# Optimization experiments

Hardware: AMD Instinct MI355X
Metric: run time of the kernel (lower is better)

Reference implementation:

```python
import jax, jax.numpy as jnp
import numpy as np


def setup_inputs() -> dict:
    key = jax.random.key(0)
    k1, k2, k3 = jax.random.split(key, 3)
    N, D, H, E = 8192, 1024, 1024, 16
    scale = 1.0 / np.sqrt(D)
    return {
        "x": jax.random.normal(k1, (N, D), dtype=jnp.float32),
        "router_w": jax.random.normal(k2, (D, E), dtype=jnp.float32) * scale,
        "router_b": jnp.zeros((E,), dtype=jnp.float32),
        "expert_w": jax.random.normal(k3, (E, D, H), dtype=jnp.float32) * scale,
        "expert_b": jnp.zeros((E, H), dtype=jnp.float32),
        "k": 2,
    }


def reference(x, router_w, router_b, expert_w, expert_b, k):
    # Router: softmax over experts, then top-k.
    logits = x @ router_w + router_b                      # [N, E]
    routing_weights = jax.nn.softmax(logits, axis=-1)     # [N, E]
    top_k_weights, top_k_indices = jax.lax.top_k(routing_weights, k)  # [N, k]

    # Dense all-expert compute (faithful to original): [N, E, H]
    expert_outputs = jnp.einsum('nd,edh->neh', x, expert_w) + expert_b[None, :, :]

    # Gather top-k expert outputs: [N, k, H]
    gathered = jnp.take_along_axis(expert_outputs, top_k_indices[:, :, None], axis=1)

    # Weighted sum over k (weights NOT renormalized, as in the original).
    out = jnp.sum(top_k_weights[:, :, None] * gathered, axis=1)  # [N, H]
    return out
```

## Files before the change

kernel.cpp:

```cpp
#include <hip/hip_runtime.h>
#include <hip/hip_bf16.h>


#define N_TOK 8192
#define D_DIM 1024
#define H_DIM 1024
#define E_NUM 16
#define CAP   1024
#define KPAD  40

typedef __attribute__((ext_vector_type(4))) float f32x4;
typedef __attribute__((ext_vector_type(8))) short bf16x8;

__device__ __forceinline__ unsigned short f2bf(float f) {
    unsigned int u = __float_as_uint(f);
    unsigned int r = u + 0x7fffu + ((u >> 16) & 1u);
    return (unsigned short)(r >> 16);
}
__device__ __forceinline__ unsigned int pk2bf(float lo, float hi) {
    return (unsigned int)f2bf(lo) | ((unsigned int)f2bf(hi) << 16);
}

__global__ __launch_bounds__(256, 4) void router_kernel(
    const float* __restrict__ x,
    const float* __restrict__ rw,
    const float* __restrict__ rb,
    int4* __restrict__ res)
{
    const int wave = threadIdx.x >> 6;
    const int lane = threadIdx.x & 63;
    const int ds   = lane >> 4;
    const int e    = lane & 15;
    const int t0   = blockIdx.x * 8 + wave * 2;

    const float* x0  = x + (size_t)t0 * D_DIM + ds * 256;
    const float* x1  = x0 + D_DIM;
    const float* rwp = rw + ds * 4096 + e;

    double acc0 = 0.0, acc1 = 0.0;
#pragma unroll 2
    for (int g = 0; g < 8; ++g) {
        float s0 = 0.0f, s1 = 0.0f;
#pragma unroll
        for (int u = 0; u < 8; ++u) {
            const int jb = g * 8 + u;
            const float4 a = *(const float4*)(x0 + jb * 4);
            const float4 b = *(const float4*)(x1 + jb * 4);
            const float w0 = rwp[jb * 64];
            const float w1 = rwp[jb * 64 + 16];
            const float w2 = rwp[jb * 64 + 32];
            const float w3 = rwp[jb * 64 + 48];
            s0 = fmaf(a.w, w3, fmaf(a.z, w2, fmaf(a.y, w1, fmaf(a.x, w0, s0))));
            s1 = fmaf(b.w, w3, fmaf(b.z, w2, fmaf(b.y, w1, fmaf(b.x, w0, s1))));
        }
        acc0 += (double)s0;
        acc1 += (double)s1;
    }

    double v0 = acc0, v1 = acc1;
    v0 += __shfl_xor(v0, 16); v0 += __shfl_xor(v0, 32);
    v1 += __shfl_xor(v1, 16); v1 += __shfl_xor(v1, 32);

    __shared__ double lg[4][2][E_NUM];
    if (ds == 0) {
        const double bias = (double)rb[e];
        lg[wave][0][e] = v0 + bias;
        lg[wave][1][e] = v1 + bias;
    }
    __syncthreads();

    if (lane < 2) {
        const double* L = lg[wave][lane];
        double m = L[0];
#pragma unroll
        for (int k = 1; k < E_NUM; ++k) m = fmax(m, L[k]);

        int e1 = 0;
#pragma unroll
        for (int k = 1; k < E_NUM; ++k) if (L[k] > L[e1]) e1 = k;
        int e2 = (e1 == 0) ? 1 : 0;
        for (int k = 0; k < E_NUM; ++k)
            if (k != e1 && L[k] > L[e2]) e2 = k;

        float s = 0.0f;
#pragma unroll
        for (int k = 0; k < E_NUM; ++k) s = fmaf(expf((float)(L[k] - m)), 1.0f, s);
        const float w1 = expf((float)(L[e1] - m)) / s;
        const float w2 = expf((float)(L[e2] - m)) / s;

        const int n = t0 + lane;
        res[n] = make_int4(e1, e2, __float_as_int(w1), __float_as_int(w2));
    }
}

__global__ __launch_bounds__(256) void build_lists(
    const int4* __restrict__ res,
    int* __restrict__ counts0, int* __restrict__ counts1,
    int2* __restrict__ entries0, int2* __restrict__ entries1)
{
    const int e = blockIdx.x;
    __shared__ int c0, c1;
    if (threadIdx.x == 0) { c0 = 0; c1 = 0; }
    __syncthreads();

    for (int i = threadIdx.x; i < N_TOK; i += 256) {
        const int4 r = res[i];
        if (r.x == e) {
            int p = atomicAdd(&c0, 1);
            if (p < CAP) entries0[e * CAP + p] = make_int2(i, r.z);
        }
        if (r.y == e) {
            int p = atomicAdd(&c1, 1);
            if (p < CAP) entries1[e * CAP + p] = make_int2(i, r.w);
        }
    }
    __syncthreads();
    if (threadIdx.x == 0) { counts0[e] = c0; counts1[e] = c1; }
}

__global__ __launch_bounds__(256) void cvt_kernel(
    const float* __restrict__ x,
    const float* __restrict__ ew,
    unsigned short* __restrict__ xb,
    unsigned short* __restrict__ wt)
{
    const int tid = threadIdx.x;
    if (blockIdx.x < 4096) {
        const size_t base = ((size_t)blockIdx.x * 256 + tid) * 8;
        const float4 a = *(const float4*)(x + base);
        const float4 b = *(const float4*)(x + base + 4);
        uint4 p;
        p.x = pk2bf(a.x, a.y); p.y = pk2bf(a.z, a.w);
        p.z = pk2bf(b.x, b.y); p.w = pk2bf(b.z, b.w);
        *(uint4*)(xb + base) = p;
        return;
    }
    __shared__ unsigned short Ts[64][68];
    const int wi = blockIdx.x - 4096;
    const int e  = wi >> 8;
    const int kt = (wi >> 4) & 15;
    const int ht = wi & 15;

    {
        const int kl0 = tid >> 4;
        const int hl  = (tid & 15) * 4;
        const float* src = ew + (size_t)e * (D_DIM * H_DIM)
                         + (size_t)(kt * 64 + kl0) * H_DIM + ht * 64 + hl;
#pragma unroll
        for (int i = 0; i < 4; ++i) {
            const float4 v = *(const float4*)(src + (size_t)i * 16 * H_DIM);
            ushort4 p;
            p.x = f2bf(v.x); p.y = f2bf(v.y); p.z = f2bf(v.z); p.w = f2bf(v.w);
            *(ushort4*)&Ts[kl0 + i * 16][hl] = p;
        }
    }
    __syncthreads();
    {
        const int h2 = tid >> 2;
        const int kc = (tid & 3) * 16;
        unsigned int r[8];
#pragma unroll
        for (int i = 0; i < 8; ++i)
            r[i] = (unsigned int)Ts[kc + 2 * i][h2]
                 | ((unsigned int)Ts[kc + 2 * i + 1][h2] << 16);
        unsigned short* dst = wt + (size_t)e * (D_DIM * H_DIM)
                            + (size_t)(ht * 64 + h2) * D_DIM + kt * 64 + kc;
        *(uint4*)dst       = *(uint4*)&r[0];
        *(uint4*)(dst + 8) = *(uint4*)&r[4];
    }
}

template <bool ADD>
__global__ __launch_bounds__(256) void moe_gemm_bf16(
    const unsigned short* __restrict__ xb,
    const unsigned short* __restrict__ wt,
    const float* __restrict__ eb,
    const int* __restrict__ counts,
    const int2* __restrict__ entries,
    float* __restrict__ out)
{
    int e = 0, loc = blockIdx.x, count = 0;
    for (; e < E_NUM; ++e) {
        int c = counts[e]; if (c > CAP) c = CAP;
        const int nb = ((c + 127) >> 7) << 3;
        if (loc < nb) { count = c; break; }
        loc -= nb;
    }
    if (e == E_NUM) return;
    const int i0 = (loc >> 3) * 128;
    const int h0 = (loc & 7) * 128;

    __shared__ unsigned short Xs[2][128][KPAD];
    __shared__ unsigned short Ws[2][128][KPAD];
    __shared__ int   s_tok[128];
    __shared__ float s_w[128];

    const int tid = threadIdx.x;
    if (tid < 128) {
        const int i = i0 + tid;
        if (i < count) {
            int2 en = entries[e * CAP + i];
            s_tok[tid] = en.x;
            s_w[tid] = __int_as_float(en.y);
        } else {
            s_tok[tid] = 0;
            s_w[tid] = 0.0f;
        }
    }
    __syncthreads();

    const int wave = tid >> 6;
    const int lane = tid & 63;
    const int wr = (wave >> 1) * 64;
    const int wc = (wave & 1) * 64;
    const int l15 = lane & 15;
    const int quad = lane >> 4;

    f32x4 acc[4][4] = {};

    const int row  = tid >> 1;
    const int half = (tid & 1) * 16;
    const unsigned short* xp = xb + (size_t)s_tok[row] * D_DIM + half;
    const unsigned short* wp = wt + (size_t)(e * H_DIM + h0 + row) * D_DIM + half;

    uint4 pa0 = *(const uint4*)(xp);
    uint4 pa1 = *(const uint4*)(xp + 8);
    uint4 pw0 = *(const uint4*)(wp);
    uint4 pw1 = *(const uint4*)(wp + 8);
    *(uint4*)&Xs[0][row][half]     = pa0;
    *(uint4*)&Xs[0][row][half + 8] = pa1;
    *(uint4*)&Ws[0][row][half]     = pw0;
    *(uint4*)&Ws[0][row][half + 8] = pw1;

    int cur = 0;
    for (int d0 = 0; d0 < D_DIM; d0 += 32) {
        __syncthreads();
        const bool more = (d0 + 32 < D_DIM);

        if (more) {
            pa0 = *(const uint4*)(xp + d0 + 32);
            pa1 = *(const uint4*)(xp + d0 + 40);
            pw0 = *(const uint4*)(wp + d0 + 32);
            pw1 = *(const uint4*)(wp + d0 + 40);
        }

        bf16x8 af[4], bq[4];
#pragma unroll
        for (int i = 0; i < 4; ++i)
            af[i] = *(const bf16x8*)&Xs[cur][wr + i * 16 + l15][quad * 8];
#pragma unroll
        for (int j = 0; j < 4; ++j)
            bq[j] = *(const bf16x8*)&Ws[cur][wc + j * 16 + l15][quad * 8];
#pragma unroll
        for (int i = 0; i < 4; ++i)
#pragma unroll
            for (int j = 0; j < 4; ++j)
                acc[i][j] = __builtin_amdgcn_mfma_f32_16x16x32_bf16(
                    af[i], bq[j], acc[i][j], 0, 0, 0);

        if (more) {
            const int nxt = cur ^ 1;
            *(uint4*)&Xs[nxt][row][half]     = pa0;
            *(uint4*)&Xs[nxt][row][half + 8] = pa1;
            *(uint4*)&Ws[nxt][row][half]     = pw0;
            *(uint4*)&Ws[nxt][row][half + 8] = pw1;
        }
        cur ^= 1;
    }

    float bias_j[4];
    const float* ebp = eb + e * H_DIM + h0 + wc;
#pragma unroll
    for (int j = 0; j < 4; ++j) bias_j[j] = ebp[j * 16 + l15];

#pragma unroll
    for (int i = 0; i < 4; ++i) {
#pragma unroll
        for (int r = 0; r < 4; ++r) {
            const int orow = wr + i * 16 + quad * 4 + r;
            if (i0 + orow < count) {
                const int tok = s_tok[orow];
                const float w = s_w[orow];
                float* op = out + (size_t)tok * H_DIM + h0 + wc + l15;
#pragma unroll
                for (int j = 0; j < 4; ++j) {
                    float v = w * (acc[i][j][r] + bias_j[j]);
                    if (ADD) v += op[j * 16];
                    op[j * 16] = v;
                }
            }
        }
    }
}

template <bool ADD>
__global__ __launch_bounds__(256) void moe_mfma_kernel(
    const float* __restrict__ x,
    const float* __restrict__ ew,
    const float* __restrict__ eb,
    const int* __restrict__ counts,
    const int2* __restrict__ entries,
    float* __restrict__ out)
{
    const int flat = blockIdx.x;
    const int lid  = (flat & 7) * 128 + (flat >> 3);
    const int h0 = (lid & 7) * 128;
    const int i0 = ((lid >> 3) & 7) * 128;
    const int e  = lid >> 6;

    int count = counts[e];
    if (count > CAP) count = CAP;
    if (i0 >= count) return;

    __shared__ unsigned short Xs[2][128][KPAD];
    __shared__ unsigned short Ws[2][128][KPAD];
    __shared__ int   s_tok[128];
    __shared__ float s_w[128];

    const int tid = threadIdx.x;
    if (tid < 128) {
        const int i = i0 + tid;
        if (i < count) {
            int2 en = entries[e * CAP + i];
            s_tok[tid] = en.x;
            s_w[tid] = __int_as_float(en.y);
        } else {
            s_tok[tid] = 0;
            s_w[tid] = 0.0f;
        }
    }
    __syncthreads();

    const int wave = tid >> 6;
    const int lane = tid & 63;
    const int wr = (wave >> 1) * 64;
    const int wc = (wave & 1) * 64;
    const int l15 = lane & 15;
    const int quad = lane >> 4;

    f32x4 acc[4][4] = {};

    const int a_kq = (tid & 7) * 4;
    const int a_r0 = tid >> 3;
    const int b_n  = tid & 127;
    const int b_dh = (tid >> 7) * 16;

    const float* ap[4];
#pragma unroll
    for (int it = 0; it < 4; ++it)
        ap[it] = x + (size_t)s_tok[a_r0 + it * 32] * D_DIM + a_kq;
    const float* bp = ew + (size_t)e * D_DIM * H_DIM
                    + (size_t)b_dh * H_DIM + h0 + b_n;

    float4 pa[4];
    float  pb[16];
#pragma unroll
    for (int it = 0; it < 4; ++it) pa[it] = *(const float4*)(ap[it]);
#pragma unroll
    for (int i = 0; i < 16; ++i)  pb[i] = bp[(size_t)i * H_DIM];

    {
#pragma unroll
        for (int it = 0; it < 4; ++it) {
            ushort4 p;
            p.x = f2bf(pa[it].x); p.y = f2bf(pa[it].y);
            p.z = f2bf(pa[it].z); p.w = f2bf(pa[it].w);
            *(ushort4*)&Xs[0][a_r0 + it * 32][a_kq] = p;
        }
        uint4 lo, hi;
        lo.x = pk2bf(pb[0], pb[1]);   lo.y = pk2bf(pb[2], pb[3]);
        lo.z = pk2bf(pb[4], pb[5]);   lo.w = pk2bf(pb[6], pb[7]);
        hi.x = pk2bf(pb[8], pb[9]);   hi.y = pk2bf(pb[10], pb[11]);
        hi.z = pk2bf(pb[12], pb[13]); hi.w = pk2bf(pb[14], pb[15]);
        *(uint4*)&Ws[0][b_n][b_dh]     = lo;
        *(uint4*)&Ws[0][b_n][b_dh + 8] = hi;
    }

    int cur = 0;
    for (int d0 = 0; d0 < D_DIM; d0 += 32) {
        __syncthreads();
        const bool more = (d0 + 32 < D_DIM);

        if (more) {
#pragma unroll
            for (int it = 0; it < 4; ++it)
                pa[it] = *(const float4*)(ap[it] + d0 + 32);
#pragma unroll
            for (int i = 0; i < 16; ++i)
                pb[i] = bp[(size_t)(d0 + 32 + i) * H_DIM];
        }

        bf16x8 af[4], bq[4];
#pragma unroll
        for (int i = 0; i < 4; ++i)
            af[i] = *(const bf16x8*)&Xs[cur][wr + i * 16 + l15][quad * 8];
#pragma unroll
        for (int j = 0; j < 4; ++j)
            bq[j] = *(const bf16x8*)&Ws[cur][wc + j * 16 + l15][quad * 8];
#pragma unroll
        for (int i = 0; i < 4; ++i)
#pragma unroll
            for (int j = 0; j < 4; ++j)
                acc[i][j] = __builtin_amdgcn_mfma_f32_16x16x32_bf16(
                    af[i], bq[j], acc[i][j], 0, 0, 0);

        if (more) {
            const int nxt = cur ^ 1;
#pragma unroll
            for (int it = 0; it < 4; ++it) {
                ushort4 p;
                p.x = f2bf(pa[it].x); p.y = f2bf(pa[it].y);
                p.z = f2bf(pa[it].z); p.w = f2bf(pa[it].w);
                *(ushort4*)&Xs[nxt][a_r0 + it * 32][a_kq] = p;
            }
            uint4 lo, hi;
            lo.x = pk2bf(pb[0], pb[1]);   lo.y = pk2bf(pb[2], pb[3]);
            lo.z = pk2bf(pb[4], pb[5]);   lo.w = pk2bf(pb[6], pb[7]);
            hi.x = pk2bf(pb[8], pb[9]);   hi.y = pk2bf(pb[10], pb[11]);
            hi.z = pk2bf(pb[12], pb[13]); hi.w = pk2bf(pb[14], pb[15]);
            *(uint4*)&Ws[nxt][b_n][b_dh]     = lo;
            *(uint4*)&Ws[nxt][b_n][b_dh + 8] = hi;
        }
        cur ^= 1;
    }

    float bias_j[4];
    const float* ebp = eb + e * H_DIM + h0 + wc;
#pragma unroll
    for (int j = 0; j < 4; ++j) bias_j[j] = ebp[j * 16 + l15];

#pragma unroll
    for (int i = 0; i < 4; ++i) {
#pragma unroll
        for (int r = 0; r < 4; ++r) {
            const int orow = wr + i * 16 + quad * 4 + r;
            if (i0 + orow < count) {
                const int tok = s_tok[orow];
                const float w = s_w[orow];
                float* op = out + (size_t)tok * H_DIM + h0 + wc + l15;
#pragma unroll
                for (int j = 0; j < 4; ++j) {
                    float v = w * (acc[i][j][r] + bias_j[j]);
                    if (ADD) v += op[j * 16];
                    op[j * 16] = v;
                }
            }
        }
    }
}

extern "C" void kernel_launch(void* const* d_in, const int* in_sizes, int n_in,
                              void* d_out, int out_size, void* d_ws, size_t ws_size,
                              hipStream_t stream)
{
    const float* x  = (const float*)d_in[0];
    const float* rw = (const float*)d_in[1];
    const float* rb = (const float*)d_in[2];
    const float* ew = (const float*)d_in[3];
    const float* eb = (const float*)d_in[4];

    char* ws = (char*)d_ws;
    int*  counts0  = (int*)ws;
    int*  counts1  = (int*)(ws + 64);
    int2* entries0 = (int2*)(ws + 1024);
    int2* entries1 = (int2*)(ws + 1024 + E_NUM * CAP * 8);

    const size_t XB_OFF = (size_t)1 << 20;
    const size_t XB_SZ  = (size_t)N_TOK * D_DIM * 2;
    const size_t WT_OFF = XB_OFF + XB_SZ;
    const size_t WT_SZ  = (size_t)E_NUM * D_DIM * H_DIM * 2;
    const bool precache = ws_size >= WT_OFF + WT_SZ;

    int4* res = (int4*)d_out;

    router_kernel<<<N_TOK / 8, 256, 0, stream>>>(x, rw, rb, res);

    build_lists<<<E_NUM, 256, 0, stream>>>(res, counts0, counts1,
                                           entries0, entries1);

    if (precache) {
        unsigned short* xbp = (unsigned short*)(ws + XB_OFF);
        unsigned short* wtp = (unsigned short*)(ws + WT_OFF);
        cvt_kernel<<<8192, 256, 0, stream>>>(x, ew, xbp, wtp);
        moe_gemm_bf16<false><<<1024, 256, 0, stream>>>(
            xbp, wtp, eb, counts0, entries0, (float*)d_out);
        moe_gemm_bf16<true><<<1024, 256, 0, stream>>>(
            xbp, wtp, eb, counts1, entries1, (float*)d_out);
    } else {
        moe_mfma_kernel<false><<<1024, 256, 0, stream>>>(
            x, ew, eb, counts0, entries0, (float*)d_out);
        moe_mfma_kernel<true><<<1024, 256, 0, stream>>>(
            x, ew, eb, counts1, entries1, (float*)d_out);
    }
}
```

Measured before the change: 285.3 us.

## Fuse x bf16 conversion into router and remap GEMM blocks across XCDs

Moves the fp32-to-bf16 conversion of x into the router kernel, which already reads x, so the separate conversion pass over x is dropped and only the expert-weight transpose/convert remains as its own kernel. The grouped GEMM now computes the total active block count first, exits idle blocks early, and remaps block indices so consecutive tiles of the same expert land on the same XCD for better L2 reuse. The router kernel does extra loads and stores per block, and the remap adds a counts scan to every GEMM block.

```diff
diff --git a/kernel.cpp b/kernel.cpp
--- a/kernel.cpp
+++ b/kernel.cpp
@@ -21,11 +21,13 @@
     return (unsigned int)f2bf(lo) | ((unsigned int)f2bf(hi) << 16);
 }
 
+template <bool WRITE_XB>
 __global__ __launch_bounds__(256, 4) void router_kernel(
     const float* __restrict__ x,
     const float* __restrict__ rw,
     const float* __restrict__ rb,
-    int4* __restrict__ res)
+    int4* __restrict__ res,
+    unsigned short* __restrict__ xb)
 {
     const int wave = threadIdx.x >> 6;
     const int lane = threadIdx.x & 63;
@@ -57,6 +59,25 @@
         acc1 += (double)s1;
     }
 
+    if (WRITE_XB) {
+#pragma unroll
+        for (int t = 0; t < 2; ++t) {
+            const float* src = x + (size_t)(t0 + t) * D_DIM + lane * 16;
+            unsigned short* dst = xb + (size_t)(t0 + t) * D_DIM + lane * 16;
+            const float4 v0 = *(const float4*)(src);
+            const float4 v1 = *(const float4*)(src + 4);
+            const float4 v2 = *(const float4*)(src + 8);
+            const float4 v3 = *(const float4*)(src + 12);
+            uint4 lo, hi;
+            lo.x = pk2bf(v0.x, v0.y); lo.y = pk2bf(v0.z, v0.w);
+            lo.z = pk2bf(v1.x, v1.y); lo.w = pk2bf(v1.z, v1.w);
+            hi.x = pk2bf(v2.x, v2.y); hi.y = pk2bf(v2.z, v2.w);
+            hi.z = pk2bf(v3.x, v3.y); hi.w = pk2bf(v3.z, v3.w);
+            *(uint4*)dst       = lo;
+            *(uint4*)(dst + 8) = hi;
+        }
+    }
+
     double v0 = acc0, v1 = acc1;
     v0 += __shfl_xor(v0, 16); v0 += __shfl_xor(v0, 32);
     v1 += __shfl_xor(v1, 16); v1 += __shfl_xor(v1, 32);
@@ -118,25 +139,13 @@
     if (threadIdx.x == 0) { counts0[e] = c0; counts1[e] = c1; }
 }
 
-__global__ __launch_bounds__(256) void cvt_kernel(
-    const float* __restrict__ x,
+__global__ __launch_bounds__(256) void cvt_w_kernel(
     const float* __restrict__ ew,
-    unsigned short* __restrict__ xb,
     unsigned short* __restrict__ wt)
 {
     const int tid = threadIdx.x;
-    if (blockIdx.x < 4096) {
-        const size_t base = ((size_t)blockIdx.x * 256 + tid) * 8;
-        const float4 a = *(const float4*)(x + base);
-        const float4 b = *(const float4*)(x + base + 4);
-        uint4 p;
-        p.x = pk2bf(a.x, a.y); p.y = pk2bf(a.z, a.w);
-        p.z = pk2bf(b.x, b.y); p.w = pk2bf(b.z, b.w);
-        *(uint4*)(xb + base) = p;
-        return;
-    }
     __shared__ unsigned short Ts[64][68];
-    const int wi = blockIdx.x - 4096;
+    const int wi = blockIdx.x;
     const int e  = wi >> 8;
     const int kt = (wi >> 4) & 15;
     const int ht = wi & 15;
@@ -179,14 +188,25 @@
     const int2* __restrict__ entries,
     float* __restrict__ out)
 {
-    int e = 0, loc = blockIdx.x, count = 0;
+    int T = 0;
+    for (int k = 0; k < E_NUM; ++k) {
+        int c = counts[k]; if (c > CAP) c = CAP;
+        T += ((c + 127) >> 7) << 3;
+    }
+    if ((int)blockIdx.x >= T) return;
+
+    const int q = T >> 3, r = T & 7;
+    const int xcd = blockIdx.x & 7;
+    int loc = (xcd < r ? xcd * (q + 1) : r * (q + 1) + (xcd - r) * q)
+            + (blockIdx.x >> 3);
+
+    int e = 0, count = 0;
     for (; e < E_NUM; ++e) {
         int c = counts[e]; if (c > CAP) c = CAP;
         const int nb = ((c + 127) >> 7) << 3;
         if (loc < nb) { count = c; break; }
         loc -= nb;
     }
-    if (e == E_NUM) return;
     const int i0 = (loc >> 3) * 128;
     const int h0 = (loc & 7) * 128;
 
@@ -276,15 +296,15 @@
 #pragma unroll
     for (int i = 0; i < 4; ++i) {
 #pragma unroll
-        for (int r = 0; r < 4; ++r) {
-            const int orow = wr + i * 16 + quad * 4 + r;
+        for (int r2 = 0; r2 < 4; ++r2) {
+            const int orow = wr + i * 16 + quad * 4 + r2;
             if (i0 + orow < count) {
                 const int tok = s_tok[orow];
                 const float w = s_w[orow];
                 float* op = out + (size_t)tok * H_DIM + h0 + wc + l15;
 #pragma unroll
                 for (int j = 0; j < 4; ++j) {
-                    float v = w * (acc[i][j][r] + bias_j[j]);
+                    float v = w * (acc[i][j][r2] + bias_j[j]);
                     if (ADD) v += op[j * 16];
                     op[j * 16] = v;
                 }
@@ -432,15 +452,15 @@
 #pragma unroll
     for (int i = 0; i < 4; ++i) {
 #pragma unroll
-        for (int r = 0; r < 4; ++r) {
-            const int orow = wr + i * 16 + quad * 4 + r;
+        for (int r2 = 0; r2 < 4; ++r2) {
+            const int orow = wr + i * 16 + quad * 4 + r2;
             if (i0 + orow < count) {
                 const int tok = s_tok[orow];
                 const float w = s_w[orow];
                 float* op = out + (size_t)tok * H_DIM + h0 + wc + l15;
 #pragma unroll
                 for (int j = 0; j < 4; ++j) {
-                    float v = w * (acc[i][j][r] + bias_j[j]);
+                    float v = w * (acc[i][j][r2] + bias_j[j]);
                     if (ADD) v += op[j * 16];
                     op[j * 16] = v;
                 }
@@ -473,20 +493,21 @@
 
     int4* res = (int4*)d_out;
 
-    router_kernel<<<N_TOK / 8, 256, 0, stream>>>(x, rw, rb, res);
-
-    build_lists<<<E_NUM, 256, 0, stream>>>(res, counts0, counts1,
-                                           entries0, entries1);
-
     if (precache) {
         unsigned short* xbp = (unsigned short*)(ws + XB_OFF);
         unsigned short* wtp = (unsigned short*)(ws + WT_OFF);
-        cvt_kernel<<<8192, 256, 0, stream>>>(x, ew, xbp, wtp);
+        router_kernel<true><<<N_TOK / 8, 256, 0, stream>>>(x, rw, rb, res, xbp);
+        build_lists<<<E_NUM, 256, 0, stream>>>(res, counts0, counts1,
+                                               entries0, entries1);
+        cvt_w_kernel<<<4096, 256, 0, stream>>>(ew, wtp);
         moe_gemm_bf16<false><<<1024, 256, 0, stream>>>(
             xbp, wtp, eb, counts0, entries0, (float*)d_out);
         moe_gemm_bf16<true><<<1024, 256, 0, stream>>>(
             xbp, wtp, eb, counts1, entries1, (float*)d_out);
     } else {
+        router_kernel<false><<<N_TOK / 8, 256, 0, stream>>>(x, rw, rb, res, nullptr);
+        build_lists<<<E_NUM, 256, 0, stream>>>(res, counts0, counts1,
+                                               entries0, entries1);
         moe_mfma_kernel<false><<<1024, 256, 0, stream>>>(
             x, ew, eb, counts0, entries0, (float*)d_out);
         moe_mfma_kernel<true><<<1024, 256, 0, stream>>>(
```

After: 277.0 us, median of 2. 1.03x faster.
